# Kernel tuning notes

Measured on AMD Instinct MI355X. Metric: run time of the kernel, lower is better.

Reference implementation:

```python
import jax, jax.numpy as jnp
import numpy as np

N = 50000      # nodes per graph (= num hyperedges, forced by the stack ops)
E = 800000     # incidence pairs per graph
L = 16         # max nodes per hyperedge (padded with index 0)
F_IN = 128     # in_channels
D1 = 256       # dim_1
D2 = D1 // 4   # conv2 out dim = FusionAttention in_size
H_ATT = 128    # FusionAttention hidden_size
EPS = 1e-15


def setup_inputs() -> dict:
    key = jax.random.key(0)
    ks = jax.random.split(key, 32)
    inp = {}
    for i in range(4):
        inp[f"x{i}"] = jax.random.normal(ks[i], (N, F_IN), jnp.float32)
        nidx = jax.random.randint(ks[4 + i], (E,), 0, N, dtype=jnp.int32)
        eidx = jax.random.randint(ks[8 + i], (E,), 0, N, dtype=jnp.int32)
        inp[f"ei{i}"] = jnp.stack([nidx, eidx])  # [2, E]
        hn = jax.random.randint(ks[12 + i], (N, L), 0, N + 1, dtype=jnp.int32)
        inp[f"hnode{i}"] = hn
        # hye_len = number of real (non-padding) entries per hyperedge
        inp[f"hlen{i}"] = jnp.sum(hn > 0, axis=1, keepdims=True).astype(jnp.float32)
    # shared Hgnn params (PyG HypergraphConv: lin without bias + separate bias)
    inp["W1"] = jax.random.normal(ks[16], (F_IN, D1), jnp.float32) / np.sqrt(F_IN).astype(np.float32)
    inp["b1"] = jnp.zeros((D1,), jnp.float32)
    inp["W2"] = jax.random.normal(ks[17], (D1, D2), jnp.float32) / np.sqrt(D1).astype(np.float32)
    inp["b2"] = jnp.zeros((D2,), jnp.float32)
    # two FusionAttention heads: Linear(D2,H_ATT)+Tanh, Linear(H_ATT,1,bias=False)
    for name, a, b in [("ac", 18, 19), ("am", 20, 21)]:
        inp[f"{name}_W1"] = jax.random.normal(ks[a], (D2, H_ATT), jnp.float32) / np.sqrt(D2).astype(np.float32)
        inp[f"{name}_b1"] = jnp.zeros((H_ATT,), jnp.float32)
        inp[f"{name}_W2"] = jax.random.normal(ks[b], (H_ATT, 1), jnp.float32) / np.sqrt(H_ATT).astype(np.float32)
    return inp


def _hconv(x, node_idx, edge_idx, W, b):
    """PyG HypergraphConv (heads=1, unit hyperedge weights):
    X' = D^-1 H B^-1 H^T (X W) + b, via two segment-sum passes."""
    x = x @ W  # [N, out]
    ones = jnp.ones(node_idx.shape, x.dtype)
    deg_n = jax.ops.segment_sum(ones, node_idx, num_segments=N)
    d_inv = jnp.where(deg_n > 0, 1.0 / deg_n, 0.0)
    deg_e = jax.ops.segment_sum(ones, edge_idx, num_segments=N)
    b_inv = jnp.where(deg_e > 0, 1.0 / deg_e, 0.0)
    # node -> hyperedge: m_e = B^-1[e] * sum_{v in e} x[v]
    efeat = b_inv[:, None] * jax.ops.segment_sum(x[node_idx], edge_idx, num_segments=N)
    # hyperedge -> node: out_v = D^-1[v] * sum_{e : v in e} m_e
    out = d_inv[:, None] * jax.ops.segment_sum(efeat[edge_idx], node_idx, num_segments=N)
    return out + b


def _hgnn(x, ei, W1, b1, W2, b2):
    x = jax.nn.relu(_hconv(x, ei[0], ei[1], W1, b1))
    return jax.nn.relu(_hconv(x, ei[0], ei[1], W2, b2))


def _hye_emb(node_emb, hlen, hnode):
    # prepend zero row so padding index 0 gathers zeros
    padded = jnp.concatenate([jnp.zeros((1, node_emb.shape[1]), node_emb.dtype), node_emb], axis=0)
    seq = padded[hnode]                    # [M, L, F]
    return jnp.sum(seq, axis=1) / (hlen + EPS)


def _fusion_attn(z, W1, b1, W2):
    # z: [N, 4, d]
    w = (jnp.tanh(z @ W1 + b1) @ W2).mean(0)      # [4, 1]
    beta = jax.nn.softmax(w, axis=0)              # [4, 1]
    return jnp.sum(beta * z, axis=1)              # [N, d]


def reference(x0, x1, x2, x3, ei0, ei1, ei2, ei3,
              hlen0, hlen1, hlen2, hlen3, hnode0, hnode1, hnode2, hnode3,
              W1, b1, W2, b2, ac_W1, ac_b1, ac_W2, am_W1, am_b1, am_W2):
    x1_cm = _hgnn(x0, ei0, W1, b1, W2, b2)
    x1_mc = _hgnn(x1, ei1, W1, b1, W2, b2)
    x1_cc = _hgnn(x2, ei2, W1, b1, W2, b2)
    x1_mm = _hgnn(x3, ei3, W1, b1, W2, b2)
    x2_cm = _hye_emb(x1_cm, hlen0, hnode0)
    x2_mc = _hye_emb(x1_mc, hlen1, hnode1)
    x2_cc = _hye_emb(x1_cc, hlen2, hnode2)
    x2_mm = _hye_emb(x1_mm, hlen3, hnode3)
    x_c = jnp.stack((x1_mc, x2_cm, x1_cc, x2_cc), axis=1)  # [N, 4, D2]
    x_m = jnp.stack((x1_cm, x2_mc, x1_mm, x2_mm), axis=1)
    h_c = _fusion_attn(x_c, ac_W1, ac_b1, ac_W2)
    h_m = _fusion_attn(x_m, am_W1, am_b1, am_W2)
    return (h_c, h_m)
```

## Files before the change

### kernel.cpp

```cpp
#include <hip/hip_runtime.h>
#include <hip/hip_bf16.h>

#define NF   128
#define DD1  256
#define DD2  64
#define HATT 128

static inline int cdiv(int a, int b) { return (a + b - 1) / b; }

__global__ __launch_bounds__(256) void count_rank(const int* __restrict__ nidx,
                                                  const int* __restrict__ eidx,
                                                  int* __restrict__ deg,
                                                  int* __restrict__ rank,
                                                  int N, int E) {
    int e = blockIdx.x * 256 + threadIdx.x;
    if (e < E) {
        const int vn = nidx[e], ve = eidx[e];
        const int rn = atomicAdd(&deg[vn], 1);
        const int re = atomicAdd(&deg[N + ve], 1);
        rank[e] = rn | (re << 16);
    }
}

__global__ __launch_bounds__(256) void scan_blocks(const int* __restrict__ in,
                                                   int* __restrict__ out,
                                                   int* __restrict__ partials, int n) {
    __shared__ int s[256];
    const int base = blockIdx.x * 1024;
    const int t = threadIdx.x;
    int v[4], sum = 0;
#pragma unroll
    for (int i = 0; i < 4; i++) {
        const int idx = base + t * 4 + i;
        v[i] = (idx < n) ? in[idx] : 0;
        sum += v[i];
    }
    s[t] = sum;
    __syncthreads();
    for (int o = 1; o < 256; o <<= 1) {
        int x = 0;
        if (t >= o) x = s[t - o];
        __syncthreads();
        if (t >= o) s[t] += x;
        __syncthreads();
    }
    if (t == 255) partials[blockIdx.x] = s[255];
    int run = (t == 0) ? 0 : s[t - 1];
#pragma unroll
    for (int i = 0; i < 4; i++) {
        const int idx = base + t * 4 + i;
        if (idx < n) out[idx] = run;
        run += v[i];
    }
}

__global__ __launch_bounds__(256) void scan_partials(int* __restrict__ partials, int P) {
    __shared__ int s[256];
    const int t = threadIdx.x;
    s[t] = (t < P) ? partials[t] : 0;
    __syncthreads();
    for (int o = 1; o < 256; o <<= 1) {
        int x = 0;
        if (t >= o) x = s[t - o];
        __syncthreads();
        if (t >= o) s[t] += x;
        __syncthreads();
    }
    if (t < P) partials[t] = (t == 0) ? 0 : s[t - 1];
}

__global__ __launch_bounds__(256) void scan_add(int* __restrict__ off,
                                                const int* __restrict__ partials,
                                                int n, int total) {
    const int idx = blockIdx.x * 256 + threadIdx.x;
    if (idx < n) off[idx] += partials[idx >> 10];
    if (idx == 0) off[n] = total;
}

__global__ __launch_bounds__(256) void build_fill(const int* __restrict__ nidx,
                                                  const int* __restrict__ eidx,
                                                  const int* __restrict__ rank,
                                                  const int* __restrict__ off,
                                                  int* __restrict__ srcidx,
                                                  int N, int E, int shardSize) {
    const int shard = blockIdx.x & 7;
    const int chunk = blockIdx.x >> 3;
    const int lo = shard * shardSize;
    const int hi = lo + shardSize;
    const int base = chunk * 1024;
#pragma unroll
    for (int i = 0; i < 4; i++) {
        const int e = base + i * 256 + threadIdx.x;
        if (e < E) {
            const int vn = nidx[e], ve = eidx[e];
            const int rk = rank[e];
            if (vn >= lo && vn < hi)
                srcidx[off[vn] + (rk & 0xffff)] = ve;
            if (ve >= lo && ve < hi)
                srcidx[off[N + ve] + (rk >> 16)] = vn;
        }
    }
}

__global__ __launch_bounds__(256) void invert_deg_int(const int* __restrict__ deg,
                                                      float* __restrict__ inv, int n) {
    int t = blockIdx.x * 256 + threadIdx.x;
    if (t < n) {
        const int v = deg[t];
        inv[t] = (v > 0) ? 1.0f / (float)v : 0.f;
    }
}

__global__ __launch_bounds__(256) void gather_rows_128(const float* __restrict__ src,
                                                       const int* __restrict__ off,
                                                       const int* __restrict__ srcidx,
                                                       const float* __restrict__ scale,
                                                       float* __restrict__ dst, int Nn) {
    const int row = blockIdx.x * 8 + (threadIdx.x >> 5);
    if (row >= Nn) return;
    const int c = (threadIdx.x & 31) << 2;
    const int j0 = off[row], j1 = off[row + 1];
    float4 a0 = make_float4(0.f, 0.f, 0.f, 0.f);
    float4 a1 = make_float4(0.f, 0.f, 0.f, 0.f);
    int j = j0;
    for (; j + 1 < j1; j += 2) {
        const int s0 = srcidx[j];
        const int s1 = srcidx[j + 1];
        const float4 v0 = *(const float4*)&src[(size_t)s0 * 128 + c];
        const float4 v1 = *(const float4*)&src[(size_t)s1 * 128 + c];
        a0.x += v0.x; a0.y += v0.y; a0.z += v0.z; a0.w += v0.w;
        a1.x += v1.x; a1.y += v1.y; a1.z += v1.z; a1.w += v1.w;
    }
    if (j < j1) {
        const int s0 = srcidx[j];
        const float4 v0 = *(const float4*)&src[(size_t)s0 * 128 + c];
        a0.x += v0.x; a0.y += v0.y; a0.z += v0.z; a0.w += v0.w;
    }
    float4 acc = make_float4(a0.x + a1.x, a0.y + a1.y, a0.z + a1.z, a0.w + a1.w);
    if (scale) {
        const float s = scale[row];
        acc.x *= s; acc.y *= s; acc.z *= s; acc.w *= s;
    }
    *(float4*)&dst[(size_t)row * 128 + c] = acc;
}

__global__ __launch_bounds__(256) void gather_rows_64(const float* __restrict__ src,
                                                      const int* __restrict__ off,
                                                      const int* __restrict__ srcidx,
                                                      const float* __restrict__ scale,
                                                      const float* __restrict__ post_bias,
                                                      float* __restrict__ dst, int Nn) {
    const int row = blockIdx.x * 16 + (threadIdx.x >> 4);
    if (row >= Nn) return;
    const int c = (threadIdx.x & 15) << 2;
    const int j0 = off[row], j1 = off[row + 1];
    float4 a0 = make_float4(0.f, 0.f, 0.f, 0.f);
    float4 a1 = make_float4(0.f, 0.f, 0.f, 0.f);
    int j = j0;
    for (; j + 1 < j1; j += 2) {
        const int s0 = srcidx[j];
        const int s1 = srcidx[j + 1];
        const float4 v0 = *(const float4*)&src[(size_t)s0 * 64 + c];
        const float4 v1 = *(const float4*)&src[(size_t)s1 * 64 + c];
        a0.x += v0.x; a0.y += v0.y; a0.z += v0.z; a0.w += v0.w;
        a1.x += v1.x; a1.y += v1.y; a1.z += v1.z; a1.w += v1.w;
    }
    if (j < j1) {
        const int s0 = srcidx[j];
        const float4 v0 = *(const float4*)&src[(size_t)s0 * 64 + c];
        a0.x += v0.x; a0.y += v0.y; a0.z += v0.z; a0.w += v0.w;
    }
    float4 acc = make_float4(a0.x + a1.x, a0.y + a1.y, a0.z + a1.z, a0.w + a1.w);
    if (scale) {
        const float s = scale[row];
        acc.x *= s; acc.y *= s; acc.z *= s; acc.w *= s;
    }
    if (post_bias) {
        acc.x = fmaxf(acc.x + post_bias[c + 0], 0.f);
        acc.y = fmaxf(acc.y + post_bias[c + 1], 0.f);
        acc.z = fmaxf(acc.z + post_bias[c + 2], 0.f);
        acc.w = fmaxf(acc.w + post_bias[c + 3], 0.f);
    }
    *(float4*)&dst[(size_t)row * 64 + c] = acc;
}

__global__ __launch_bounds__(256) void gemm1_f32(const float* __restrict__ A,
                                                 const float* __restrict__ B,
                                                 float* __restrict__ C, int M,
                                                 const float* __restrict__ dinv,
                                                 const float* __restrict__ bias) {
    __shared__ float As[32][132];
    __shared__ float Bs[32][128];
    const int tid = threadIdx.x;
    const int m0 = blockIdx.y * 128;
    const int bn = blockIdx.x * 128;
    const int tr = (tid >> 4) << 3;
    const int tc = (tid & 15) << 3;

    float acc[8][8] = {{0.f}};

    for (int k0 = 0; k0 < 128; k0 += 32) {
#pragma unroll
        for (int i = 0; i < 4; i++) {
            const int f = tid + 256 * i;
            const int r = f >> 3;
            const int q = (f & 7) << 2;
            const int grow = m0 + r;
            float4 v = make_float4(0.f, 0.f, 0.f, 0.f);
            if (grow < M) v = *(const float4*)&A[(size_t)grow * 128 + k0 + q];
            As[q + 0][r] = v.x;
            As[q + 1][r] = v.y;
            As[q + 2][r] = v.z;
            As[q + 3][r] = v.w;
        }
#pragma unroll
        for (int i = 0; i < 4; i++) {
            const int f = tid + 256 * i;
            const int r = f >> 5;
            const int c4 = (f & 31) << 2;
            *(float4*)&Bs[r][c4] = *(const float4*)&B[(size_t)(k0 + r) * 256 + bn + c4];
        }
        __syncthreads();
#pragma unroll
        for (int k = 0; k < 32; k++) {
            float av[8], bv[8];
            *(float4*)&av[0] = *(const float4*)&As[k][tr];
            *(float4*)&av[4] = *(const float4*)&As[k][tr + 4];
            *(float4*)&bv[0] = *(const float4*)&Bs[k][tc];
            *(float4*)&bv[4] = *(const float4*)&Bs[k][tc + 4];
#pragma unroll
            for (int r = 0; r < 8; r++)
#pragma unroll
                for (int c = 0; c < 8; c++)
                    acc[r][c] = fmaf(av[r], bv[c], acc[r][c]);
        }
        __syncthreads();
    }
#pragma unroll
    for (int r = 0; r < 8; r++) {
        const int grow = m0 + tr + r;
        if (grow < M) {
            const float s = dinv[grow];
            float o[8];
#pragma unroll
            for (int c = 0; c < 8; c++)
                o[c] = fmaxf(fmaf(acc[r][c], s, bias[bn + tc + c]), 0.f);
            *(float4*)&C[(size_t)grow * 256 + bn + tc] = *(float4*)&o[0];
            *(float4*)&C[(size_t)grow * 256 + bn + tc + 4] = *(float4*)&o[4];
        }
    }
}

__global__ __launch_bounds__(256) void gemm2_f32(const float* __restrict__ A,
                                                 const float* __restrict__ B,
                                                 float* __restrict__ C, int M) {
    __shared__ float As[32][132];
    __shared__ float Bs[32][64];
    const int tid = threadIdx.x;
    const int m0 = blockIdx.y * 128;
    const int tr = (tid >> 3) << 2;
    const int tc = (tid & 7) << 3;

    float acc[4][8] = {{0.f}};

    for (int k0 = 0; k0 < 256; k0 += 32) {
#pragma unroll
        for (int i = 0; i < 4; i++) {
            const int f = tid + 256 * i;
            const int r = f >> 3;
            const int q = (f & 7) << 2;
            const int grow = m0 + r;
            float4 v = make_float4(0.f, 0.f, 0.f, 0.f);
            if (grow < M) v = *(const float4*)&A[(size_t)grow * 256 + k0 + q];
            As[q + 0][r] = v.x;
            As[q + 1][r] = v.y;
            As[q + 2][r] = v.z;
            As[q + 3][r] = v.w;
        }
#pragma unroll
        for (int i = 0; i < 2; i++) {
            const int f = tid + 256 * i;
            const int r = f >> 4;
            const int c4 = (f & 15) << 2;
            *(float4*)&Bs[r][c4] = *(const float4*)&B[(size_t)(k0 + r) * 64 + c4];
        }
        __syncthreads();
#pragma unroll
        for (int k = 0; k < 32; k++) {
            float av[4], bv[8];
            *(float4*)&av[0] = *(const float4*)&As[k][tr];
            *(float4*)&bv[0] = *(const float4*)&Bs[k][tc];
            *(float4*)&bv[4] = *(const float4*)&Bs[k][tc + 4];
#pragma unroll
            for (int r = 0; r < 4; r++)
#pragma unroll
                for (int c = 0; c < 8; c++)
                    acc[r][c] = fmaf(av[r], bv[c], acc[r][c]);
        }
        __syncthreads();
    }
#pragma unroll
    for (int r = 0; r < 4; r++) {
        const int grow = m0 + tr + r;
        if (grow < M) {
            *(float4*)&C[(size_t)grow * 64 + tc] =
                make_float4(acc[r][0], acc[r][1], acc[r][2], acc[r][3]);
            *(float4*)&C[(size_t)grow * 64 + tc + 4] =
                make_float4(acc[r][4], acc[r][5], acc[r][6], acc[r][7]);
        }
    }
}

__global__ __launch_bounds__(256) void hye_emb_kernel(const float* __restrict__ emb,
                                                      const int* __restrict__ hnode,
                                                      const float* __restrict__ hlen,
                                                      float* __restrict__ out, int Nn) {
    const int r = blockIdx.x * 16 + (threadIdx.x >> 4);
    const int c = (threadIdx.x & 15) << 2;
    if (r >= Nn) return;
    const int* hp = &hnode[(size_t)r * 16];
    float4 acc = make_float4(0.f, 0.f, 0.f, 0.f);
#pragma unroll
    for (int l = 0; l < 16; l++) {
        const int idx = hp[l];
        if (idx > 0) {
            const float4 v = *(const float4*)&emb[(size_t)(idx - 1) * 64 + c];
            acc.x += v.x; acc.y += v.y; acc.z += v.z; acc.w += v.w;
        }
    }
    const float inv = 1.0f / (hlen[r] + 1e-15f);
    acc.x *= inv; acc.y *= inv; acc.z *= inv; acc.w *= inv;
    *(float4*)&out[(size_t)r * 64 + c] = acc;
}

struct AttnArgs {
    const float* z[8];
    const float* W1c; const float* b1c; const float* W2c;
    const float* W1m; const float* b1m; const float* W2m;
    float* accw;
    int Nn;
};

__global__ __launch_bounds__(256) void attn_gemm(AttnArgs a) {
    __shared__ float As[64][132];
    __shared__ float Bs[64][128];
    __shared__ float red[4];
    const int tid = threadIdx.x;
    const int gy = blockIdx.y;
    const int head = gy >> 2;
    const float* __restrict__ z  = a.z[gy];
    const float* __restrict__ W1 = head ? a.W1m : a.W1c;
    const float* __restrict__ b1 = head ? a.b1m : a.b1c;
    const float* __restrict__ W2 = head ? a.W2m : a.W2c;
    const int m0 = blockIdx.x * 128;

    {
        const int c4 = tid & 15;
        const int mb = tid >> 4;
#pragma unroll
        for (int i = 0; i < 8; i++) {
            const int m = mb + 16 * i;
            const int grow = m0 + m;
            float4 v = make_float4(0.f, 0.f, 0.f, 0.f);
            if (grow < a.Nn) v = *(const float4*)&z[(size_t)grow * 64 + c4 * 4];
            As[c4 * 4 + 0][m] = v.x;
            As[c4 * 4 + 1][m] = v.y;
            As[c4 * 4 + 2][m] = v.z;
            As[c4 * 4 + 3][m] = v.w;
        }
    }
    {
#pragma unroll
        for (int i = 0; i < 8; i++) {
            const int f = tid + 256 * i;
            const int r = f >> 5, cc = (f & 31) << 2;
            *(float4*)&Bs[r][cc] = *(const float4*)&W1[(size_t)r * 128 + cc];
        }
    }
    __syncthreads();

    const int tr = (tid & 15) * 8;
    const int tc = (tid >> 4) * 8;
    float acc[8][8] = {{0.f}};
    for (int k = 0; k < 64; k++) {
        float av[8], bv[8];
        *(float4*)&av[0] = *(const float4*)&As[k][tr];
        *(float4*)&av[4] = *(const float4*)&As[k][tr + 4];
        *(float4*)&bv[0] = *(const float4*)&Bs[k][tc];
        *(float4*)&bv[4] = *(const float4*)&Bs[k][tc + 4];
#pragma unroll
        for (int r = 0; r < 8; r++)
#pragma unroll
            for (int c = 0; c < 8; c++)
                acc[r][c] = fmaf(av[r], bv[c], acc[r][c]);
    }

    float w2v[8], b1v[8];
#pragma unroll
    for (int c = 0; c < 8; c++) { w2v[c] = W2[tc + c]; b1v[c] = b1[tc + c]; }
    float local = 0.f;
#pragma unroll
    for (int r = 0; r < 8; r++) {
        if (m0 + tr + r < a.Nn) {
#pragma unroll
            for (int c = 0; c < 8; c++) {
                float s = acc[r][c] + b1v[c];
                s = fminf(fmaxf(s, -15.f), 15.f);
                const float t = __expf(2.f * s);
                local += (1.f - 2.f / (t + 1.f)) * w2v[c];
            }
        }
    }
#pragma unroll
    for (int off = 32; off >= 1; off >>= 1) local += __shfl_down(local, off, 64);
    if ((tid & 63) == 0) red[tid >> 6] = local;
    __syncthreads();
    if (tid == 0) atomicAdd(&a.accw[gy], red[0] + red[1] + red[2] + red[3]);
}

__global__ void softmax_beta(const float* __restrict__ acc, float* __restrict__ beta,
                             float invN) {
    const int t = threadIdx.x;
    if (t < 2) {
        const float* a = acc + 4 * t;
        float* b = beta + 4 * t;
        float w[4], m = -1e30f;
#pragma unroll
        for (int i = 0; i < 4; i++) { w[i] = a[i] * invN; m = fmaxf(m, w[i]); }
        float s = 0.f;
#pragma unroll
        for (int i = 0; i < 4; i++) { w[i] = expf(w[i] - m); s += w[i]; }
#pragma unroll
        for (int i = 0; i < 4; i++) b[i] = w[i] / s;
    }
}

__global__ __launch_bounds__(256) void weighted_sum(const float* __restrict__ z0,
                                                    const float* __restrict__ z1,
                                                    const float* __restrict__ z2,
                                                    const float* __restrict__ z3,
                                                    const float* __restrict__ beta,
                                                    float* __restrict__ out, int Nn) {
    const int t = blockIdx.x * 256 + threadIdx.x;
    if (t >= Nn * 16) return;
    const float b0 = beta[0], b1 = beta[1], b2 = beta[2], b3 = beta[3];
    const float4 v0 = *(const float4*)&z0[(size_t)t * 4];
    const float4 v1 = *(const float4*)&z1[(size_t)t * 4];
    const float4 v2 = *(const float4*)&z2[(size_t)t * 4];
    const float4 v3 = *(const float4*)&z3[(size_t)t * 4];
    float4 o;
    o.x = b0 * v0.x + b1 * v1.x + b2 * v2.x + b3 * v3.x;
    o.y = b0 * v0.y + b1 * v1.y + b2 * v2.y + b3 * v3.y;
    o.z = b0 * v0.z + b1 * v1.z + b2 * v2.z + b3 * v3.z;
    o.w = b0 * v0.w + b1 * v1.w + b2 * v2.w + b3 * v3.w;
    *(float4*)&out[(size_t)t * 4] = o;
}

extern "C" void kernel_launch(void* const* d_in, const int* in_sizes, int n_in,
                              void* d_out, int out_size, void* d_ws, size_t ws_size,
                              hipStream_t stream) {
    const int Nn = in_sizes[0] / NF;
    const int E  = in_sizes[1] / 2;
    const int N2 = 2 * Nn;

    const float* x[4];
    const int*   ei[4];
    const int*   hnode[4];
    const float* hlen[4];
    for (int g = 0; g < 4; g++) {
        x[g]     = (const float*)d_in[4 * g + 0];
        ei[g]    = (const int*)d_in[4 * g + 1];
        hnode[g] = (const int*)d_in[4 * g + 2];
        hlen[g]  = (const float*)d_in[4 * g + 3];
    }
    const float* W1   = (const float*)d_in[16];
    const float* b1   = (const float*)d_in[17];
    const float* W2   = (const float*)d_in[18];
    const float* b2   = (const float*)d_in[19];
    const float* acW1 = (const float*)d_in[20];
    const float* acb1 = (const float*)d_in[21];
    const float* acW2 = (const float*)d_in[22];
    const float* amW1 = (const float*)d_in[23];
    const float* amb1 = (const float*)d_in[24];
    const float* amW2 = (const float*)d_in[25];

    float* ws = (float*)d_ws;
    size_t o = 0;
    float* bufA = ws + o; o += (size_t)Nn * DD1;
    float* bufB = ws + o; o += (size_t)Nn * DD1;
    float* dinv = ws + o; o += N2;
    float* h2[4];
    float* hemb[4];
    for (int g = 0; g < 4; g++) { h2[g]   = ws + o; o += (size_t)Nn * DD2; }
    for (int g = 0; g < 4; g++) { hemb[g] = ws + o; o += (size_t)Nn * DD2; }
    float* accw = ws + o; o += 8;
    float* beta = ws + o; o += 8;
    int* iws = (int*)(ws + o);
    size_t io = 0;
    int* deg_i    = iws + io; io += N2;
    int* off      = iws + io; io += N2 + 1;
    int* partials = iws + io; io += 256;
    int* rank     = iws + io; io += E;
    int* srcidx   = iws + io; io += (size_t)2 * E;

    const int nScanBlocks = cdiv(N2, 1024);
    const int shardSize = cdiv(Nn, 8);

    for (int g = 0; g < 4; g++) {
        const int* nidx = ei[g];
        const int* eidx = ei[g] + E;
        const int* off_n = off;
        const int* off_e = off + Nn;
        const float* d_inv = dinv;
        const float* b_inv = dinv + Nn;

        hipMemsetAsync(deg_i, 0, (size_t)N2 * sizeof(int), stream);
        count_rank<<<cdiv(E, 256), 256, 0, stream>>>(nidx, eidx, deg_i, rank, Nn, E);
        scan_blocks<<<nScanBlocks, 256, 0, stream>>>(deg_i, off, partials, N2);
        scan_partials<<<1, 256, 0, stream>>>(partials, nScanBlocks);
        scan_add<<<cdiv(N2, 256), 256, 0, stream>>>(off, partials, N2, 2 * E);
        build_fill<<<8 * cdiv(E, 1024), 256, 0, stream>>>(nidx, eidx, rank, off,
                                                          srcidx, Nn, E, shardSize);
        invert_deg_int<<<cdiv(N2, 256), 256, 0, stream>>>(deg_i, dinv, N2);

        gather_rows_128<<<cdiv(Nn, 8), 256, 0, stream>>>(x[g], off_e, srcidx, b_inv, bufB, Nn);
        gather_rows_128<<<cdiv(Nn, 8), 256, 0, stream>>>(bufB, off_n, srcidx, nullptr, bufA, Nn);
        gemm1_f32<<<dim3(2, cdiv(Nn, 128)), 256, 0, stream>>>(bufA, W1, bufB, Nn, d_inv, b1);

        gemm2_f32<<<dim3(1, cdiv(Nn, 128)), 256, 0, stream>>>(bufB, W2, bufA, Nn);
        gather_rows_64<<<cdiv(Nn, 16), 256, 0, stream>>>(bufA, off_e, srcidx, b_inv,
                                                         nullptr, bufB, Nn);
        gather_rows_64<<<cdiv(Nn, 16), 256, 0, stream>>>(bufB, off_n, srcidx, d_inv,
                                                         b2, h2[g], Nn);

        hye_emb_kernel<<<cdiv(Nn, 16), 256, 0, stream>>>(h2[g], hnode[g], hlen[g], hemb[g], Nn);
    }

    hipMemsetAsync(accw, 0, 8 * sizeof(float), stream);
    AttnArgs aa;
    aa.z[0] = h2[1]; aa.z[1] = hemb[0]; aa.z[2] = h2[2]; aa.z[3] = hemb[2];
    aa.z[4] = h2[0]; aa.z[5] = hemb[1]; aa.z[6] = h2[3]; aa.z[7] = hemb[3];
    aa.W1c = acW1; aa.b1c = acb1; aa.W2c = acW2;
    aa.W1m = amW1; aa.b1m = amb1; aa.W2m = amW2;
    aa.accw = accw; aa.Nn = Nn;
    attn_gemm<<<dim3(cdiv(Nn, 128), 8), 256, 0, stream>>>(aa);
    softmax_beta<<<1, 64, 0, stream>>>(accw, beta, 1.0f / (float)Nn);

    float* out = (float*)d_out;
    weighted_sum<<<cdiv(Nn * 16, 256), 256, 0, stream>>>(h2[1], hemb[0], h2[2], hemb[2],
                                                         beta + 0, out, Nn);
    weighted_sum<<<cdiv(Nn * 16, 256), 256, 0, stream>>>(h2[0], hemb[1], h2[3], hemb[3],
                                                         beta + 4, out + (size_t)Nn * DD2, Nn);
}
```

Measured before the change: 1.905 ms.

## Unroll gather loops to four accumulators and remap GEMM thread tiles to strided quads

The CSR gather kernels now keep four independent accumulators with a 4-way unrolled loop, and hye_emb uses two accumulators, so more independent loads are in flight per thread. The gemm1 and attention GEMM kernels change each thread's 8x8 register tile from a contiguous 8-wide block to two 4-wide quads spaced 64 apart. This is meant to cut LDS bank conflicts on the float4 shared-memory reads and make stores more coalesced. The extra accumulators raise register pressure, and summation order changes slightly.

```diff
diff --git a/kernel.cpp b/kernel.cpp
--- a/kernel.cpp
+++ b/kernel.cpp
@@ -122,21 +122,30 @@
     const int j0 = off[row], j1 = off[row + 1];
     float4 a0 = make_float4(0.f, 0.f, 0.f, 0.f);
     float4 a1 = make_float4(0.f, 0.f, 0.f, 0.f);
+    float4 a2 = make_float4(0.f, 0.f, 0.f, 0.f);
+    float4 a3 = make_float4(0.f, 0.f, 0.f, 0.f);
     int j = j0;
-    for (; j + 1 < j1; j += 2) {
-        const int s0 = srcidx[j];
+    for (; j + 3 < j1; j += 4) {
+        const int s0 = srcidx[j + 0];
         const int s1 = srcidx[j + 1];
+        const int s2 = srcidx[j + 2];
+        const int s3 = srcidx[j + 3];
         const float4 v0 = *(const float4*)&src[(size_t)s0 * 128 + c];
         const float4 v1 = *(const float4*)&src[(size_t)s1 * 128 + c];
+        const float4 v2 = *(const float4*)&src[(size_t)s2 * 128 + c];
+        const float4 v3 = *(const float4*)&src[(size_t)s3 * 128 + c];
         a0.x += v0.x; a0.y += v0.y; a0.z += v0.z; a0.w += v0.w;
         a1.x += v1.x; a1.y += v1.y; a1.z += v1.z; a1.w += v1.w;
-    }
-    if (j < j1) {
+        a2.x += v2.x; a2.y += v2.y; a2.z += v2.z; a2.w += v2.w;
+        a3.x += v3.x; a3.y += v3.y; a3.z += v3.z; a3.w += v3.w;
+    }
+    for (; j < j1; j++) {
         const int s0 = srcidx[j];
         const float4 v0 = *(const float4*)&src[(size_t)s0 * 128 + c];
         a0.x += v0.x; a0.y += v0.y; a0.z += v0.z; a0.w += v0.w;
     }
-    float4 acc = make_float4(a0.x + a1.x, a0.y + a1.y, a0.z + a1.z, a0.w + a1.w);
+    float4 acc = make_float4(a0.x + a1.x + a2.x + a3.x, a0.y + a1.y + a2.y + a3.y,
+                             a0.z + a1.z + a2.z + a3.z, a0.w + a1.w + a2.w + a3.w);
     if (scale) {
         const float s = scale[row];
         acc.x *= s; acc.y *= s; acc.z *= s; acc.w *= s;
@@ -156,21 +165,30 @@
     const int j0 = off[row], j1 = off[row + 1];
     float4 a0 = make_float4(0.f, 0.f, 0.f, 0.f);
     float4 a1 = make_float4(0.f, 0.f, 0.f, 0.f);
+    float4 a2 = make_float4(0.f, 0.f, 0.f, 0.f);
+    float4 a3 = make_float4(0.f, 0.f, 0.f, 0.f);
     int j = j0;
-    for (; j + 1 < j1; j += 2) {
-        const int s0 = srcidx[j];
+    for (; j + 3 < j1; j += 4) {
+        const int s0 = srcidx[j + 0];
         const int s1 = srcidx[j + 1];
+        const int s2 = srcidx[j + 2];
+        const int s3 = srcidx[j + 3];
         const float4 v0 = *(const float4*)&src[(size_t)s0 * 64 + c];
         const float4 v1 = *(const float4*)&src[(size_t)s1 * 64 + c];
+        const float4 v2 = *(const float4*)&src[(size_t)s2 * 64 + c];
+        const float4 v3 = *(const float4*)&src[(size_t)s3 * 64 + c];
         a0.x += v0.x; a0.y += v0.y; a0.z += v0.z; a0.w += v0.w;
         a1.x += v1.x; a1.y += v1.y; a1.z += v1.z; a1.w += v1.w;
-    }
-    if (j < j1) {
+        a2.x += v2.x; a2.y += v2.y; a2.z += v2.z; a2.w += v2.w;
+        a3.x += v3.x; a3.y += v3.y; a3.z += v3.z; a3.w += v3.w;
+    }
+    for (; j < j1; j++) {
         const int s0 = srcidx[j];
         const float4 v0 = *(const float4*)&src[(size_t)s0 * 64 + c];
         a0.x += v0.x; a0.y += v0.y; a0.z += v0.z; a0.w += v0.w;
     }
-    float4 acc = make_float4(a0.x + a1.x, a0.y + a1.y, a0.z + a1.z, a0.w + a1.w);
+    float4 acc = make_float4(a0.x + a1.x + a2.x + a3.x, a0.y + a1.y + a2.y + a3.y,
+                             a0.z + a1.z + a2.z + a3.z, a0.w + a1.w + a2.w + a3.w);
     if (scale) {
         const float s = scale[row];
         acc.x *= s; acc.y *= s; acc.z *= s; acc.w *= s;
@@ -194,8 +212,8 @@
     const int tid = threadIdx.x;
     const int m0 = blockIdx.y * 128;
     const int bn = blockIdx.x * 128;
-    const int tr = (tid >> 4) << 3;
-    const int tc = (tid & 15) << 3;
+    const int rq = (tid >> 4) << 2;
+    const int cq = (tid & 15) << 2;
 
     float acc[8][8] = {{0.f}};
 
@@ -224,10 +242,10 @@
 #pragma unroll
         for (int k = 0; k < 32; k++) {
             float av[8], bv[8];
-            *(float4*)&av[0] = *(const float4*)&As[k][tr];
-            *(float4*)&av[4] = *(const float4*)&As[k][tr + 4];
-            *(float4*)&bv[0] = *(const float4*)&Bs[k][tc];
-            *(float4*)&bv[4] = *(const float4*)&Bs[k][tc + 4];
+            *(float4*)&av[0] = *(const float4*)&As[k][rq];
+            *(float4*)&av[4] = *(const float4*)&As[k][rq + 64];
+            *(float4*)&bv[0] = *(const float4*)&Bs[k][cq];
+            *(float4*)&bv[4] = *(const float4*)&Bs[k][cq + 64];
 #pragma unroll
             for (int r = 0; r < 8; r++)
 #pragma unroll
@@ -238,15 +256,18 @@
     }
 #pragma unroll
     for (int r = 0; r < 8; r++) {
-        const int grow = m0 + tr + r;
+        const int grow = m0 + rq + (r & 3) + ((r >> 2) << 6);
         if (grow < M) {
             const float s = dinv[grow];
             float o[8];
 #pragma unroll
-            for (int c = 0; c < 8; c++)
-                o[c] = fmaxf(fmaf(acc[r][c], s, bias[bn + tc + c]), 0.f);
-            *(float4*)&C[(size_t)grow * 256 + bn + tc] = *(float4*)&o[0];
-            *(float4*)&C[(size_t)grow * 256 + bn + tc + 4] = *(float4*)&o[4];
+            for (int c = 0; c < 4; c++)
+                o[c] = fmaxf(fmaf(acc[r][c], s, bias[bn + cq + c]), 0.f);
+#pragma unroll
+            for (int c = 4; c < 8; c++)
+                o[c] = fmaxf(fmaf(acc[r][c], s, bias[bn + 64 + cq + (c - 4)]), 0.f);
+            *(float4*)&C[(size_t)grow * 256 + bn + cq] = *(float4*)&o[0];
+            *(float4*)&C[(size_t)grow * 256 + bn + 64 + cq] = *(float4*)&o[4];
         }
     }
 }
@@ -319,17 +340,26 @@
     const int c = (threadIdx.x & 15) << 2;
     if (r >= Nn) return;
     const int* hp = &hnode[(size_t)r * 16];
-    float4 acc = make_float4(0.f, 0.f, 0.f, 0.f);
-#pragma unroll
-    for (int l = 0; l < 16; l++) {
-        const int idx = hp[l];
-        if (idx > 0) {
-            const float4 v = *(const float4*)&emb[(size_t)(idx - 1) * 64 + c];
-            acc.x += v.x; acc.y += v.y; acc.z += v.z; acc.w += v.w;
+    float4 a0 = make_float4(0.f, 0.f, 0.f, 0.f);
+    float4 a1 = make_float4(0.f, 0.f, 0.f, 0.f);
+#pragma unroll
+    for (int l = 0; l < 16; l += 2) {
+        const int i0 = hp[l], i1 = hp[l + 1];
+        if (i0 > 0) {
+            const float4 v = *(const float4*)&emb[(size_t)(i0 - 1) * 64 + c];
+            a0.x += v.x; a0.y += v.y; a0.z += v.z; a0.w += v.w;
+        }
+        if (i1 > 0) {
+            const float4 v = *(const float4*)&emb[(size_t)(i1 - 1) * 64 + c];
+            a1.x += v.x; a1.y += v.y; a1.z += v.z; a1.w += v.w;
         }
     }
     const float inv = 1.0f / (hlen[r] + 1e-15f);
-    acc.x *= inv; acc.y *= inv; acc.z *= inv; acc.w *= inv;
+    float4 acc;
+    acc.x = (a0.x + a1.x) * inv;
+    acc.y = (a0.y + a1.y) * inv;
+    acc.z = (a0.z + a1.z) * inv;
+    acc.w = (a0.w + a1.w) * inv;
     *(float4*)&out[(size_t)r * 64 + c] = acc;
 }
 
@@ -379,15 +409,15 @@
     }
     __syncthreads();
 
-    const int tr = (tid & 15) * 8;
-    const int tc = (tid >> 4) * 8;
+    const int mq = (tid & 15) << 2;
+    const int hq = (tid >> 4) << 2;
     float acc[8][8] = {{0.f}};
     for (int k = 0; k < 64; k++) {
         float av[8], bv[8];
-        *(float4*)&av[0] = *(const float4*)&As[k][tr];
-        *(float4*)&av[4] = *(const float4*)&As[k][tr + 4];
-        *(float4*)&bv[0] = *(const float4*)&Bs[k][tc];
-        *(float4*)&bv[4] = *(const float4*)&Bs[k][tc + 4];
+        *(float4*)&av[0] = *(const float4*)&As[k][mq];
+        *(float4*)&av[4] = *(const float4*)&As[k][mq + 64];
+        *(float4*)&bv[0] = *(const float4*)&Bs[k][hq];
+        *(float4*)&bv[4] = *(const float4*)&Bs[k][hq + 64];
 #pragma unroll
         for (int r = 0; r < 8; r++)
 #pragma unroll
@@ -397,11 +427,16 @@
 
     float w2v[8], b1v[8];
 #pragma unroll
-    for (int c = 0; c < 8; c++) { w2v[c] = W2[tc + c]; b1v[c] = b1[tc + c]; }
+    for (int c = 0; c < 8; c++) {
+        const int col = hq + (c & 3) + ((c >> 2) << 6);
+        w2v[c] = W2[col];
+        b1v[c] = b1[col];
+    }
     float local = 0.f;
 #pragma unroll
     for (int r = 0; r < 8; r++) {
-        if (m0 + tr + r < a.Nn) {
+        const int row = m0 + mq + (r & 3) + ((r >> 2) << 6);
+        if (row < a.Nn) {
 #pragma unroll
             for (int c = 0; c < 8; c++) {
                 float s = acc[r][c] + b1v[c];
```

Result: no change. 1.883 ms (-1.2%).
